# Kernel tuning notes

Hardware: AMD Instinct MI355X
Metric: run time of the kernel (lower is better)

## Reference

```python
import jax, jax.numpy as jnp
import numpy as np

N_MODELS, N_SAMPLES, DIM = 16, 16384, 512

def setup_inputs() -> dict:
    key = jax.random.key(0)
    x = jax.random.normal(key, (N_MODELS, N_SAMPLES, DIM), dtype=jnp.float32)
    return {"x": x}

def reference(x):
    # x: [K, B, D] -> Gram-Schmidt over the K axis, per batch element.
    x1 = jnp.transpose(x, (1, 0, 2))  # [B, K, D]
    K = x1.shape[1]
    first = x1[:, 0, :]  # [B, D]
    basis = [first / jnp.linalg.norm(first, axis=1, keepdims=True)]
    for i in range(1, K):  # K is small & static; loop is over models, not data
        v = x1[:, i, :]  # [B, D]
        Bcur = jnp.stack(basis, axis=1)  # [B, i, D]
        coeffs = jnp.einsum('bd,bkd->bk', v, Bcur)  # projections onto basis
        w = v - jnp.einsum('bk,bkd->bd', coeffs, Bcur)
        w = w / jnp.linalg.norm(w, axis=1, keepdims=True)
        basis.append(w)
    return jnp.stack(basis, axis=0)  # [K, B, D]
```

## Files before the change

### kernel.cpp

```cpp
#include <hip/hip_runtime.h>
#include <utility>

#define NM 16
#define NS 16384
#define DIMV 512

template <typename F, int... Is>
__device__ __forceinline__ void sf_impl(F&& f, std::integer_sequence<int, Is...>) {
    (f(std::integral_constant<int, Is>{}), ...);
}
template <int N, typename F>
__device__ __forceinline__ void static_for(F&& f) {
    sf_impl(static_cast<F&&>(f), std::make_integer_sequence<int, N>{});
}

__global__ __launch_bounds__(256, 2) void ortho_gs_kernel(const float* __restrict__ x,
                                                          float* __restrict__ out) {
    const int gtid = blockIdx.x * blockDim.x + threadIdx.x;
    const int s    = gtid >> 6;
    const int lane = threadIdx.x & 63;
    if (s >= NS) return;

    float v[NM][8];

    static_for<NM>([&](auto M) {
        constexpr int m = M.value;
        const float4* p = (const float4*)(x + (size_t)m * (size_t)NS * DIMV
                                            + (size_t)s * DIMV);
        float4 a = p[lane];
        float4 b = p[64 + lane];
        v[m][0] = a.x; v[m][1] = a.y; v[m][2] = a.z; v[m][3] = a.w;
        v[m][4] = b.x; v[m][5] = b.y; v[m][6] = b.z; v[m][7] = b.w;
    });

    static_for<NM>([&](auto I) {
        constexpr int i = I.value;
        float c[NM > 1 ? NM : 1];
        static_for<NM>([&](auto J) {
            constexpr int j = J.value;
            if constexpr (j < i) {
                float p = 0.f;
                static_for<8>([&](auto E) {
                    constexpr int e = E.value;
                    p = fmaf(v[i][e], v[j][e], p);
                });
                c[j] = p;
            }
        });
        static_for<6>([&](auto ST) {
            constexpr int st = 1 << ST.value;
            static_for<NM>([&](auto J) {
                constexpr int j = J.value;
                if constexpr (j < i) c[j] += __shfl_xor(c[j], st, 64);
            });
        });
        static_for<NM>([&](auto J) {
            constexpr int j = J.value;
            if constexpr (j < i) {
                static_for<8>([&](auto E) {
                    constexpr int e = E.value;
                    v[i][e] = fmaf(-c[j], v[j][e], v[i][e]);
                });
            }
        });
        float n = 0.f;
        static_for<8>([&](auto E) {
            constexpr int e = E.value;
            n = fmaf(v[i][e], v[i][e], n);
        });
        static_for<6>([&](auto ST) {
            constexpr int st = 1 << ST.value;
            n += __shfl_xor(n, st, 64);
        });
        const float inv = 1.0f / sqrtf(n);
        static_for<8>([&](auto E) {
            constexpr int e = E.value;
            v[i][e] *= inv;
        });
    });

    static_for<NM>([&](auto M) {
        constexpr int m = M.value;
        float4* p = (float4*)(out + (size_t)m * (size_t)NS * DIMV
                                  + (size_t)s * DIMV);
        p[lane]      = make_float4(v[m][0], v[m][1], v[m][2], v[m][3]);
        p[64 + lane] = make_float4(v[m][4], v[m][5], v[m][6], v[m][7]);
    });
}

extern "C" void kernel_launch(void* const* d_in, const int* in_sizes, int n_in,
                              void* d_out, int out_size, void* d_ws, size_t ws_size,
                              hipStream_t stream) {
    const float* x = (const float*)d_in[0];
    float* out = (float*)d_out;
    const int threads = 256;
    const int waves_per_block = threads / 64;
    const int blocks = (NS + waves_per_block - 1) / waves_per_block;
    ortho_gs_kernel<<<blocks, threads, 0, stream>>>(x, out);
}
```

Before: 878.9 us.

## Split each sample across two waves with LDS cross-wave reductions

```diff
diff --git a/kernel.cpp b/kernel.cpp
--- a/kernel.cpp
+++ b/kernel.cpp
@@ -14,57 +14,72 @@
     sf_impl(static_cast<F&&>(f), std::make_integer_sequence<int, N>{});
 }
 
-__global__ __launch_bounds__(256, 2) void ortho_gs_kernel(const float* __restrict__ x,
+__global__ __launch_bounds__(256, 4) void ortho_gs_kernel(const float* __restrict__ x,
                                                           float* __restrict__ out) {
-    const int gtid = blockIdx.x * blockDim.x + threadIdx.x;
-    const int s    = gtid >> 6;
-    const int lane = threadIdx.x & 63;
-    if (s >= NS) return;
+    const int tid  = threadIdx.x;
+    const int lane = tid & 63;
+    const int w    = (tid >> 6) & 1;
+    const int sLoc = tid >> 7;
+    const int s    = blockIdx.x * 2 + sLoc;
 
-    float v[NM][8];
+    __shared__ float redD[2][2][NM][2];
+    __shared__ float redN[2][2][2];
+
+    float v[NM][4];
 
     static_for<NM>([&](auto M) {
         constexpr int m = M.value;
         const float4* p = (const float4*)(x + (size_t)m * (size_t)NS * DIMV
                                             + (size_t)s * DIMV);
-        float4 a = p[lane];
-        float4 b = p[64 + lane];
+        float4 a = p[w * 64 + lane];
         v[m][0] = a.x; v[m][1] = a.y; v[m][2] = a.z; v[m][3] = a.w;
-        v[m][4] = b.x; v[m][5] = b.y; v[m][6] = b.z; v[m][7] = b.w;
     });
 
     static_for<NM>([&](auto I) {
         constexpr int i = I.value;
-        float c[NM > 1 ? NM : 1];
-        static_for<NM>([&](auto J) {
-            constexpr int j = J.value;
-            if constexpr (j < i) {
+        constexpr int par = i & 1;
+
+        if constexpr (i > 0) {
+            float c[i];
+            static_for<i>([&](auto J) {
+                constexpr int j = J.value;
                 float p = 0.f;
-                static_for<8>([&](auto E) {
+                static_for<4>([&](auto E) {
                     constexpr int e = E.value;
                     p = fmaf(v[i][e], v[j][e], p);
                 });
                 c[j] = p;
+            });
+            static_for<6>([&](auto ST) {
+                constexpr int st = 1 << ST.value;
+                static_for<i>([&](auto J) {
+                    constexpr int j = J.value;
+                    c[j] += __shfl_xor(c[j], st, 64);
+                });
+            });
+            if (lane == 0) {
+                static_for<i>([&](auto J) {
+                    constexpr int j = J.value;
+                    redD[par][sLoc][j][w] = c[j];
+                });
             }
-        });
-        static_for<6>([&](auto ST) {
-            constexpr int st = 1 << ST.value;
-            static_for<NM>([&](auto J) {
+            __syncthreads();
+            static_for<i>([&](auto J) {
                 constexpr int j = J.value;
-                if constexpr (j < i) c[j] += __shfl_xor(c[j], st, 64);
+                float2 t = *(const float2*)&redD[par][sLoc][j][0];
+                c[j] = t.x + t.y;
             });
-        });
-        static_for<NM>([&](auto J) {
-            constexpr int j = J.value;
-            if constexpr (j < i) {
-                static_for<8>([&](auto E) {
+            static_for<i>([&](auto J) {
+                constexpr int j = J.value;
+                static_for<4>([&](auto E) {
                     constexpr int e = E.value;
                     v[i][e] = fmaf(-c[j], v[j][e], v[i][e]);
                 });
-            }
-        });
+            });
+        }
+
         float n = 0.f;
-        static_for<8>([&](auto E) {
+        static_for<4>([&](auto E) {
             constexpr int e = E.value;
             n = fmaf(v[i][e], v[i][e], n);
         });
@@ -72,8 +87,14 @@
             constexpr int st = 1 << ST.value;
             n += __shfl_xor(n, st, 64);
         });
+        if (lane == 0) redN[par][sLoc][w] = n;
+        __syncthreads();
+        {
+            float2 t = *(const float2*)&redN[par][sLoc][0];
+            n = t.x + t.y;
+        }
         const float inv = 1.0f / sqrtf(n);
-        static_for<8>([&](auto E) {
+        static_for<4>([&](auto E) {
             constexpr int e = E.value;
             v[i][e] *= inv;
         });
@@ -83,8 +104,7 @@
         constexpr int m = M.value;
         float4* p = (float4*)(out + (size_t)m * (size_t)NS * DIMV
                                   + (size_t)s * DIMV);
-        p[lane]      = make_float4(v[m][0], v[m][1], v[m][2], v[m][3]);
-        p[64 + lane] = make_float4(v[m][4], v[m][5], v[m][6], v[m][7]);
+        p[w * 64 + lane] = make_float4(v[m][0], v[m][1], v[m][2], v[m][3]);
     });
 }
 
@@ -94,7 +114,6 @@
     const float* x = (const float*)d_in[0];
     float* out = (float*)d_out;
     const int threads = 256;
-    const int waves_per_block = threads / 64;
-    const int blocks = (NS + waves_per_block - 1) / waves_per_block;
+    const int blocks = NS / 2;
     ortho_gs_kernel<<<blocks, threads, 0, stream>>>(x, out);
 }
```

Result: slower. 953.9 us (+8.5%).

## Replace sequential Gram-Schmidt with Gram matrix plus in-wave Cholesky factorization

Applied to the files above, without the earlier changes.

```diff
diff --git a/kernel.cpp b/kernel.cpp
--- a/kernel.cpp
+++ b/kernel.cpp
@@ -14,8 +14,8 @@
     sf_impl(static_cast<F&&>(f), std::make_integer_sequence<int, N>{});
 }
 
-__global__ __launch_bounds__(256, 2) void ortho_gs_kernel(const float* __restrict__ x,
-                                                          float* __restrict__ out) {
+__global__ __launch_bounds__(256, 2) void ortho_chol_kernel(const float* __restrict__ x,
+                                                            float* __restrict__ out) {
     const int gtid = blockIdx.x * blockDim.x + threadIdx.x;
     const int s    = gtid >> 6;
     const int lane = threadIdx.x & 63;
@@ -33,49 +33,67 @@
         v[m][4] = b.x; v[m][5] = b.y; v[m][6] = b.z; v[m][7] = b.w;
     });
 
+    float g[NM];
+    static_for<NM>([&](auto J) { g[J.value] = 0.f; });
+
     static_for<NM>([&](auto I) {
         constexpr int i = I.value;
-        float c[NM > 1 ? NM : 1];
-        static_for<NM>([&](auto J) {
+        float c[i + 1];
+        static_for<i + 1>([&](auto J) {
             constexpr int j = J.value;
-            if constexpr (j < i) {
-                float p = 0.f;
-                static_for<8>([&](auto E) {
-                    constexpr int e = E.value;
-                    p = fmaf(v[i][e], v[j][e], p);
-                });
-                c[j] = p;
-            }
+            float p = 0.f;
+            static_for<8>([&](auto E) {
+                constexpr int e = E.value;
+                p = fmaf(v[i][e], v[j][e], p);
+            });
+            c[j] = p;
         });
         static_for<6>([&](auto ST) {
             constexpr int st = 1 << ST.value;
-            static_for<NM>([&](auto J) {
+            static_for<i + 1>([&](auto J) {
                 constexpr int j = J.value;
-                if constexpr (j < i) c[j] += __shfl_xor(c[j], st, 64);
+                c[j] += __shfl_xor(c[j], st, 64);
             });
         });
+        if (lane == i) {
+            static_for<i + 1>([&](auto J) {
+                constexpr int j = J.value;
+                g[j] = c[j];
+            });
+        }
+    });
+
+    static_for<NM>([&](auto K) {
+        constexpr int k = K.value;
+        const float skk = __shfl(g[k], k, 64);
+        const float inv = 1.0f / sqrtf(skk);
+        if (lane >= k) g[k] *= inv;
         static_for<NM>([&](auto J) {
             constexpr int j = J.value;
-            if constexpr (j < i) {
-                static_for<8>([&](auto E) {
-                    constexpr int e = E.value;
-                    v[i][e] = fmaf(-c[j], v[j][e], v[i][e]);
-                });
+            if constexpr (j > k) {
+                const float Ljk = __shfl(g[k], j, 64);
+                if (lane >= j) g[j] = fmaf(-g[k], Ljk, g[j]);
             }
         });
-        float n = 0.f;
+    });
+
+    static_for<NM>([&](auto I) {
+        constexpr int i = I.value;
+        const float Lii = __shfl(g[i], i, 64);
+        const float inv = 1.0f / Lii;
+        float coef[i > 0 ? i : 1];
+        static_for<i>([&](auto J) {
+            constexpr int j = J.value;
+            coef[j] = __shfl(g[j], i, 64);
+        });
         static_for<8>([&](auto E) {
             constexpr int e = E.value;
-            n = fmaf(v[i][e], v[i][e], n);
-        });
-        static_for<6>([&](auto ST) {
-            constexpr int st = 1 << ST.value;
-            n += __shfl_xor(n, st, 64);
-        });
-        const float inv = 1.0f / sqrtf(n);
-        static_for<8>([&](auto E) {
-            constexpr int e = E.value;
-            v[i][e] *= inv;
+            float a = v[i][e];
+            static_for<i>([&](auto J) {
+                constexpr int j = J.value;
+                a = fmaf(-coef[j], v[j][e], a);
+            });
+            v[i][e] = a * inv;
         });
     });
 
@@ -96,5 +114,5 @@
     const int threads = 256;
     const int waves_per_block = threads / 64;
     const int blocks = (NS + waves_per_block - 1) / waves_per_block;
-    ortho_gs_kernel<<<blocks, threads, 0, stream>>>(x, out);
+    ortho_chol_kernel<<<blocks, threads, 0, stream>>>(x, out);
 }
```

Result: slower. 922.6 us (+5.0%).
